# Performance work log

Measured on AMD Instinct MI355X. Metric: run time of the kernel, lower is better.

Reference implementation:

```python
import jax, jax.numpy as jnp
import numpy as np

B, T_Q, T_C = 4, 2048, 2048
Q_DIM = C_DIM = H_DIM = OUT_DIM = 1024
N_HEADS = 16
D = H_DIM // N_HEADS


def setup_inputs() -> dict:
    key = jax.random.key(0)
    ks = jax.random.split(key, 10)
    s_q = 1.0 / np.sqrt(Q_DIM)
    s_c = 1.0 / np.sqrt(C_DIM)
    s_h = 1.0 / np.sqrt(H_DIM)
    return {
        "query": jax.random.normal(ks[0], (B, T_Q, Q_DIM), jnp.float32),
        "context": jax.random.normal(ks[1], (B, T_C, C_DIM), jnp.float32),
        "Wq": jax.random.uniform(ks[2], (Q_DIM, H_DIM), jnp.float32, -s_q, s_q),
        "bq": jax.random.uniform(ks[3], (H_DIM,), jnp.float32, -s_q, s_q),
        "Wk": jax.random.uniform(ks[4], (C_DIM, H_DIM), jnp.float32, -s_c, s_c),
        "bk": jax.random.uniform(ks[5], (H_DIM,), jnp.float32, -s_c, s_c),
        "Wv": jax.random.uniform(ks[6], (C_DIM, H_DIM), jnp.float32, -s_c, s_c),
        "bv": jax.random.uniform(ks[7], (H_DIM,), jnp.float32, -s_c, s_c),
        "Wo": jax.random.uniform(ks[8], (H_DIM, OUT_DIM), jnp.float32, -s_h, s_h),
        "bo": jax.random.uniform(ks[9], (OUT_DIM,), jnp.float32, -s_h, s_h),
    }


def reference(query, context, Wq, bq, Wk, bk, Wv, bv, Wo, bo):
    Bq, Tq, _ = query.shape
    _, Tc, _ = context.shape
    # project and split heads: [B, H, T, D]
    q = (query @ Wq + bq).reshape(Bq, Tq, N_HEADS, D).transpose(0, 2, 1, 3)
    k = (context @ Wk + bk).reshape(Bq, Tc, N_HEADS, D).transpose(0, 2, 1, 3)
    v = (context @ Wv + bv).reshape(Bq, Tc, N_HEADS, D).transpose(0, 2, 1, 3)
    scores = jnp.einsum("bhqd,bhkd->bhqk", q, k) / jnp.sqrt(jnp.float32(D))
    probs = jax.nn.softmax(scores, axis=-1)
    attn = jnp.einsum("bhqk,bhkd->bhqd", probs, v)  # dropout p=0 -> identity
    attn = attn.transpose(0, 2, 1, 3).reshape(Bq, Tq, N_HEADS * D)
    return attn @ Wo + bo
```

## Files before the change

kernel.cpp:

```cpp
#include <hip/hip_runtime.h>
#include <hip/hip_bf16.h>
#include <cstdint>

typedef __attribute__((ext_vector_type(8))) short short8;
typedef __attribute__((ext_vector_type(4))) short short4_t;
typedef __attribute__((ext_vector_type(4))) float f32x4;

#define MFMA16(a, b, c) __builtin_amdgcn_mfma_f32_16x16x32_bf16(a, b, c, 0, 0, 0)

__device__ __forceinline__ short f2b(float f) {
    union { float fp; unsigned u; } un; un.fp = f;
    unsigned r = un.u + 0x7fffu + ((un.u >> 16) & 1u);
    return (short)(r >> 16);
}

#if __has_builtin(__builtin_amdgcn_cvt_pk_bf16_f32)
__device__ __forceinline__ unsigned pk_bf16(float a, float b) {
    auto r = __builtin_amdgcn_cvt_pk_bf16_f32(a, b);
    unsigned u; __builtin_memcpy(&u, &r, 4); return u;
}
#else
__device__ __forceinline__ unsigned pk_bf16(float a, float b) {
    return (unsigned)(unsigned short)f2b(a) | ((unsigned)(unsigned short)f2b(b) << 16);
}
#endif

typedef const __attribute__((address_space(1))) unsigned g_as1;
typedef __attribute__((address_space(3))) unsigned l_as3;
__device__ __forceinline__ void gll16(const ushort* g, ushort* l) {
    __builtin_amdgcn_global_load_lds((g_as1*)g, (l_as3*)l, 16, 0, 0);
}

__global__ __launch_bounds__(256) void in_cvt_kernel(
    const float* __restrict__ q, const float* __restrict__ c,
    ushort* __restrict__ qb, ushort* __restrict__ cb)
{
    const float* src = blockIdx.y ? c : q;
    ushort* dst = blockIdx.y ? cb : qb;
    size_t i = ((size_t)blockIdx.x * 256 + threadIdx.x) * 8;
    float4 v0 = *(const float4*)&src[i];
    float4 v1 = *(const float4*)&src[i + 4];
    uint4 o;
    o.x = pk_bf16(v0.x, v0.y); o.y = pk_bf16(v0.z, v0.w);
    o.z = pk_bf16(v1.x, v1.y); o.w = pk_bf16(v1.z, v1.w);
    *(uint4*)&dst[i] = o;
}

__global__ __launch_bounds__(256) void wt_cvt_kernel(
    const float* __restrict__ Wq, const float* __restrict__ Wk,
    const float* __restrict__ Wv, const float* __restrict__ Wo,
    ushort* __restrict__ wt)
{
    __shared__ float Ts[64 * 65];
    const int z = blockIdx.z;
    const float* W = (z == 0) ? Wq : (z == 1) ? Wk : (z == 2) ? Wv : Wo;
    ushort* WT = wt + (size_t)z * (1024 * 1024);
    const int n0 = blockIdx.x * 64, k0 = blockIdx.y * 64;
    const int tid = threadIdx.x;

#pragma unroll
    for (int rr = 0; rr < 4; ++rr) {
        int u = tid + rr * 256;
        int r = u >> 4, c = (u & 15) * 4;
        float4 v = *(const float4*)&W[(size_t)(k0 + r) * 1024 + n0 + c];
        Ts[r * 65 + c + 0] = v.x; Ts[r * 65 + c + 1] = v.y;
        Ts[r * 65 + c + 2] = v.z; Ts[r * 65 + c + 3] = v.w;
    }
    __syncthreads();
#pragma unroll
    for (int rr = 0; rr < 4; ++rr) {
        int u = tid + rr * 256;
        int rn = u >> 4, ck = (u & 15) * 4;
        short4_t o;
        o[0] = f2b(Ts[(ck + 0) * 65 + rn]);
        o[1] = f2b(Ts[(ck + 1) * 65 + rn]);
        o[2] = f2b(Ts[(ck + 2) * 65 + rn]);
        o[3] = f2b(Ts[(ck + 3) * 65 + rn]);
        *(short4_t*)&WT[(size_t)(n0 + rn) * 1024 + k0 + ck] = o;
    }
}

template <int MODE>
__global__ __launch_bounds__(256) void gemm_kernel(
    const ushort* __restrict__ Ag, const ushort* __restrict__ BT,
    const float* __restrict__ bias, void* __restrict__ Outp, float scale)
{
    __shared__ ushort As[128 * 64];
    __shared__ ushort Bs[128 * 64];
    const int tid = threadIdx.x;
    const int w = tid >> 6, lane = tid & 63;
    const int ln = tid & 15, quad = (tid >> 4) & 3;
    const int wm = w >> 1, wn = w & 1;
    const int m0 = blockIdx.y * 128, n0 = blockIdx.x * 128;

    int offA[4], offB[4], lseg[4];
#pragma unroll
    for (int rr = 0; rr < 4; ++rr) {
        int idx = (rr * 4 + w) * 64 + lane;
        int r = idx >> 3, cst = idx & 7, csrc = cst ^ (r & 7);
        offA[rr] = (m0 + r) * 1024 + csrc * 8;
        offB[rr] = (n0 + r) * 1024 + csrc * 8;
        lseg[rr] = (rr * 4 + w) * 512;
    }

    f32x4 acc[4][4] = {};

    for (int kk = 0; kk < 1024; kk += 64) {
        __syncthreads();
#pragma unroll
        for (int rr = 0; rr < 4; ++rr)
            gll16(&Ag[(size_t)(offA[rr] + kk)], &As[lseg[rr]]);
#pragma unroll
        for (int rr = 0; rr < 4; ++rr)
            gll16(&BT[(size_t)(offB[rr] + kk)], &Bs[lseg[rr]]);
        __syncthreads();

#pragma unroll
        for (int ks = 0; ks < 2; ++ks) {
            short8 af[4], bfr[4];
#pragma unroll
            for (int i = 0; i < 4; ++i)
                af[i] = *(const short8*)&As[(wm * 64 + i * 16 + ln) * 64 +
                                            ((ks * 4 + quad) ^ (ln & 7)) * 8];
#pragma unroll
            for (int j = 0; j < 4; ++j)
                bfr[j] = *(const short8*)&Bs[(wn * 64 + j * 16 + ln) * 64 +
                                             ((ks * 4 + quad) ^ (ln & 7)) * 8];
#pragma unroll
            for (int i = 0; i < 4; ++i)
#pragma unroll
                for (int j = 0; j < 4; ++j)
                    acc[i][j] = MFMA16(af[i], bfr[j], acc[i][j]);
        }
    }

#pragma unroll
    for (int j = 0; j < 4; ++j) {
        int n = n0 + wn * 64 + j * 16 + ln;
        float bv = bias[n];
#pragma unroll
        for (int i = 0; i < 4; ++i) {
            int mb = m0 + wm * 64 + i * 16 + quad * 4;
            if (MODE == 3) {
                float* Out = (float*)Outp;
#pragma unroll
                for (int r = 0; r < 4; ++r)
                    Out[(size_t)(mb + r) * 1024 + n] = acc[i][j][r] + bv;
            } else if (MODE == 0) {
                ushort* Out = (ushort*)Outp;
                int h = n >> 6, d = n & 63;
#pragma unroll
                for (int r = 0; r < 4; ++r) {
                    int m = mb + r, b = m >> 11, t = m & 2047;
                    Out[(((size_t)(b * 16 + h) * 2048 + t) << 6) + d] =
                        (ushort)f2b((acc[i][j][r] + bv) * scale);
                }
            } else {
                ushort* Out = (ushort*)Outp;
                int h = n >> 6, d = n & 63;
                int b = mb >> 11, t = mb & 2047;
                short4_t o;
                o[0] = f2b(acc[i][j][0] + bv); o[1] = f2b(acc[i][j][1] + bv);
                o[2] = f2b(acc[i][j][2] + bv); o[3] = f2b(acc[i][j][3] + bv);
                *(short4_t*)&Out[((size_t)((b * 16 + h) * 64 + d) << 11) + t] = o;
            }
        }
    }
}

__global__ __launch_bounds__(256, 4) void attn_kernel(
    const ushort* __restrict__ Qw, const ushort* __restrict__ Kw,
    const ushort* __restrict__ Vtw, ushort* __restrict__ attn)
{
    __shared__ ushort Ks[64 * 64];
    __shared__ ushort Vts[64 * 64];
    __shared__ ushort Ps[128 * 64];
    __shared__ float red[128];

    const int tid = threadIdx.x;
    const int w = tid >> 6, lane = tid & 63;
    const int ln = tid & 15, quad = (tid >> 4) & 3;
    const int bh = blockIdx.y, b = bh >> 4, h = bh & 15;
    const int qt = blockIdx.x;

    const ushort* Qg = Qw + (size_t)bh * 131072 + (size_t)qt * 8192;
    const ushort* Kg = Kw + (size_t)bh * 131072;
    const ushort* Vg = Vtw + (size_t)bh * 131072;

    short8 bq[2][2];
#pragma unroll
    for (int qs = 0; qs < 2; ++qs)
#pragma unroll
        for (int ks = 0; ks < 2; ++ks)
            bq[qs][ks] = *(const short8*)&Qg[(w * 32 + qs * 16 + ln) * 64 + ks * 32 + quad * 8];

    int offK[2], offV[2], lseg[2];
#pragma unroll
    for (int rr = 0; rr < 2; ++rr) {
        int idx = (rr * 4 + w) * 64 + lane;
        int r = idx >> 3, cst = idx & 7, csrc = cst ^ (r & 7);
        offK[rr] = r * 64 + csrc * 8;
        offV[rr] = r * 2048 + csrc * 8;
        lseg[rr] = (rr * 4 + w) * 512;
    }

    f32x4 Of[2][4] = {};
    float psum[2] = {0.f, 0.f};

    for (int kt = 0; kt < 32; ++kt) {
        __syncthreads();
#pragma unroll
        for (int rr = 0; rr < 2; ++rr)
            gll16(&Kg[kt * 4096 + offK[rr]], &Ks[lseg[rr]]);
#pragma unroll
        for (int rr = 0; rr < 2; ++rr)
            gll16(&Vg[kt * 64 + offV[rr]], &Vts[lseg[rr]]);
        __syncthreads();

        f32x4 sa[4][2];
#pragma unroll
        for (int kv = 0; kv < 4; ++kv) {
            short8 a0 = *(const short8*)&Ks[(kv * 16 + ln) * 64 + (quad ^ (ln & 7)) * 8];
            short8 a1 = *(const short8*)&Ks[(kv * 16 + ln) * 64 + ((4 + quad) ^ (ln & 7)) * 8];
#pragma unroll
            for (int qs = 0; qs < 2; ++qs) {
                f32x4 s = {};
                s = MFMA16(a0, bq[qs][0], s);
                s = MFMA16(a1, bq[qs][1], s);
                sa[kv][qs] = s;
            }
        }

#pragma unroll
        for (int qs = 0; qs < 2; ++qs) {
            int qrow = w * 32 + qs * 16 + ln;
#pragma unroll
            for (int kv = 0; kv < 4; ++kv) {
                float p0 = __builtin_amdgcn_exp2f(sa[kv][qs][0]);
                float p1 = __builtin_amdgcn_exp2f(sa[kv][qs][1]);
                float p2 = __builtin_amdgcn_exp2f(sa[kv][qs][2]);
                float p3 = __builtin_amdgcn_exp2f(sa[kv][qs][3]);
                psum[qs] += (p0 + p1) + (p2 + p3);
                uint2 pk2;
                pk2.x = pk_bf16(p0, p1);
                pk2.y = pk_bf16(p2, p3);
                int c = 2 * kv + (quad >> 1);
                *(uint2*)&Ps[qrow * 64 + ((c ^ (ln & 7)) * 8) + (quad & 1) * 4] = pk2;
            }
        }

#pragma unroll
        for (int ks = 0; ks < 2; ++ks) {
            short8 vb[4];
#pragma unroll
            for (int ds = 0; ds < 4; ++ds)
                vb[ds] = *(const short8*)&Vts[(ds * 16 + ln) * 64 +
                                              ((ks * 4 + quad) ^ (ln & 7)) * 8];
#pragma unroll
            for (int qs = 0; qs < 2; ++qs) {
                short8 pa = *(const short8*)&Ps[(w * 32 + qs * 16 + ln) * 64 +
                                                ((ks * 4 + quad) ^ (ln & 7)) * 8];
#pragma unroll
                for (int ds = 0; ds < 4; ++ds)
                    Of[qs][ds] = MFMA16(pa, vb[ds], Of[qs][ds]);
            }
        }
    }

#pragma unroll
    for (int qs = 0; qs < 2; ++qs) {
        float l = psum[qs];
        l += __shfl_xor(l, 16);
        l += __shfl_xor(l, 32);
        if (quad == 0) red[w * 32 + qs * 16 + ln] = __builtin_amdgcn_rcpf(l);
    }

#pragma unroll
    for (int qs = 0; qs < 2; ++qs) {
        f32x4 inv = *(const f32x4*)&red[w * 32 + qs * 16 + quad * 4];
#pragma unroll
        for (int ds = 0; ds < 4; ++ds) {
#pragma unroll
            for (int r = 0; r < 4; ++r) {
                int t = qt * 128 + w * 32 + qs * 16 + quad * 4 + r;
                int col = h * 64 + ds * 16 + ln;
                attn[((size_t)(b * 2048 + t) << 10) + col] =
                    (ushort)f2b(Of[qs][ds][r] * inv[r]);
            }
        }
    }
}

extern "C" void kernel_launch(void* const* d_in, const int* in_sizes, int n_in,
                              void* d_out, int out_size, void* d_ws, size_t ws_size,
                              hipStream_t stream)
{
    const float* query   = (const float*)d_in[0];
    const float* context = (const float*)d_in[1];
    const float* Wq = (const float*)d_in[2];
    const float* bq = (const float*)d_in[3];
    const float* Wk = (const float*)d_in[4];
    const float* bk = (const float*)d_in[5];
    const float* Wv = (const float*)d_in[6];
    const float* bv = (const float*)d_in[7];
    const float* Wo = (const float*)d_in[8];
    const float* bo = (const float*)d_in[9];

    char* ws = (char*)d_ws;
    ushort* WT  = (ushort*)ws;
    ushort* Qb  = (ushort*)(ws + 8388608);
    ushort* Qw  = (ushort*)(ws + 25165824);
    ushort* Kw  = (ushort*)(ws + 41943040);
    ushort* Vtw = (ushort*)(ws + 58720256);
    ushort* Aw  = Qb;
    ushort* Cb  = (ushort*)d_out;

    const float SCALE = 0.18033688011112042f;

    in_cvt_kernel<<<dim3(4096, 2), 256, 0, stream>>>(query, context, Qb, Cb);
    wt_cvt_kernel<<<dim3(16, 16, 4), 256, 0, stream>>>(Wq, Wk, Wv, Wo, WT);
    gemm_kernel<0><<<dim3(8, 64), 256, 0, stream>>>(Qb, WT + 0 * 1048576, bq, Qw, SCALE);
    gemm_kernel<0><<<dim3(8, 64), 256, 0, stream>>>(Cb, WT + 1 * 1048576, bk, Kw, 1.0f);
    gemm_kernel<2><<<dim3(8, 64), 256, 0, stream>>>(Cb, WT + 2 * 1048576, bv, Vtw, 1.0f);
    attn_kernel<<<dim3(16, 64), 256, 0, stream>>>(Qw, Kw, Vtw, Aw);
    gemm_kernel<3><<<dim3(8, 64), 256, 0, stream>>>(Aw, WT + 3 * 1048576, bo, d_out, 1.0f);
}
```

Before: 332.2 us.

## Double-buffer K/V tiles in attention and fuse K/V projection launches

The attention kernel now double-buffers its K and V^T shared-memory tiles. It prefetches the next tile with async global-to-LDS loads while computing on the current one, which leaves a single barrier per iteration and hides load latency. The K and V projections are merged into one kv_kernel launch that selects weights and output layout by block index, saving a launch and sharing the context input. The larger shared-memory footprint lowers the attention occupancy hint from 4 to 3 blocks, and an explicit barrier is added before reading the reduction buffer.

```diff
diff --git a/kernel.cpp b/kernel.cpp
--- a/kernel.cpp
+++ b/kernel.cpp
@@ -146,7 +146,7 @@
 #pragma unroll
                 for (int r = 0; r < 4; ++r)
                     Out[(size_t)(mb + r) * 1024 + n] = acc[i][j][r] + bv;
-            } else if (MODE == 0) {
+            } else {
                 ushort* Out = (ushort*)Outp;
                 int h = n >> 6, d = n & 63;
 #pragma unroll
@@ -155,25 +155,106 @@
                     Out[(((size_t)(b * 16 + h) * 2048 + t) << 6) + d] =
                         (ushort)f2b((acc[i][j][r] + bv) * scale);
                 }
-            } else {
-                ushort* Out = (ushort*)Outp;
-                int h = n >> 6, d = n & 63;
+            }
+        }
+    }
+}
+
+__global__ __launch_bounds__(256) void kv_kernel(
+    const ushort* __restrict__ Cb, const ushort* __restrict__ WTk,
+    const ushort* __restrict__ WTv,
+    const float* __restrict__ bk, const float* __restrict__ bv,
+    ushort* __restrict__ Kw, ushort* __restrict__ Vtw)
+{
+    __shared__ ushort As[128 * 64];
+    __shared__ ushort Bs[128 * 64];
+    const int tid = threadIdx.x;
+    const int w = tid >> 6, lane = tid & 63;
+    const int ln = tid & 15, quad = (tid >> 4) & 3;
+    const int wm = w >> 1, wn = w & 1;
+    const int z = blockIdx.x >> 3;
+    const int n0 = (blockIdx.x & 7) * 128;
+    const int m0 = blockIdx.y * 128;
+    const ushort* BT = z ? WTv : WTk;
+
+    int offA[4], offB[4], lseg[4];
+#pragma unroll
+    for (int rr = 0; rr < 4; ++rr) {
+        int idx = (rr * 4 + w) * 64 + lane;
+        int r = idx >> 3, cst = idx & 7, csrc = cst ^ (r & 7);
+        offA[rr] = (m0 + r) * 1024 + csrc * 8;
+        offB[rr] = (n0 + r) * 1024 + csrc * 8;
+        lseg[rr] = (rr * 4 + w) * 512;
+    }
+
+    f32x4 acc[4][4] = {};
+
+    for (int kk = 0; kk < 1024; kk += 64) {
+        __syncthreads();
+#pragma unroll
+        for (int rr = 0; rr < 4; ++rr)
+            gll16(&Cb[(size_t)(offA[rr] + kk)], &As[lseg[rr]]);
+#pragma unroll
+        for (int rr = 0; rr < 4; ++rr)
+            gll16(&BT[(size_t)(offB[rr] + kk)], &Bs[lseg[rr]]);
+        __syncthreads();
+
+#pragma unroll
+        for (int ks = 0; ks < 2; ++ks) {
+            short8 af[4], bfr[4];
+#pragma unroll
+            for (int i = 0; i < 4; ++i)
+                af[i] = *(const short8*)&As[(wm * 64 + i * 16 + ln) * 64 +
+                                            ((ks * 4 + quad) ^ (ln & 7)) * 8];
+#pragma unroll
+            for (int j = 0; j < 4; ++j)
+                bfr[j] = *(const short8*)&Bs[(wn * 64 + j * 16 + ln) * 64 +
+                                             ((ks * 4 + quad) ^ (ln & 7)) * 8];
+#pragma unroll
+            for (int i = 0; i < 4; ++i)
+#pragma unroll
+                for (int j = 0; j < 4; ++j)
+                    acc[i][j] = MFMA16(af[i], bfr[j], acc[i][j]);
+        }
+    }
+
+#pragma unroll
+    for (int j = 0; j < 4; ++j) {
+        int n = n0 + wn * 64 + j * 16 + ln;
+        int h = n >> 6, d = n & 63;
+        if (z == 0) {
+            float bvv = bk[n];
+#pragma unroll
+            for (int i = 0; i < 4; ++i) {
+                int mb = m0 + wm * 64 + i * 16 + quad * 4;
+#pragma unroll
+                for (int r = 0; r < 4; ++r) {
+                    int m = mb + r, b = m >> 11, t = m & 2047;
+                    Kw[(((size_t)(b * 16 + h) * 2048 + t) << 6) + d] =
+                        (ushort)f2b(acc[i][j][r] + bvv);
+                }
+            }
+        } else {
+            float bvv = bv[n];
+#pragma unroll
+            for (int i = 0; i < 4; ++i) {
+                int mb = m0 + wm * 64 + i * 16 + quad * 4;
                 int b = mb >> 11, t = mb & 2047;
                 short4_t o;
-                o[0] = f2b(acc[i][j][0] + bv); o[1] = f2b(acc[i][j][1] + bv);
-                o[2] = f2b(acc[i][j][2] + bv); o[3] = f2b(acc[i][j][3] + bv);
-                *(short4_t*)&Out[((size_t)((b * 16 + h) * 64 + d) << 11) + t] = o;
-            }
-        }
-    }
-}
-
-__global__ __launch_bounds__(256, 4) void attn_kernel(
+                o[0] = f2b(acc[i][j][0] + bvv); o[1] = f2b(acc[i][j][1] + bvv);
+                o[2] = f2b(acc[i][j][2] + bvv); o[3] = f2b(acc[i][j][3] + bvv);
+                *(short4_t*)&Vtw[(((size_t)((b * 16 + h) * 64 + d)) << 11) + t] = o;
+            }
+        }
+    }
+}
+
+__global__ __launch_bounds__(256, 3) void attn_kernel(
     const ushort* __restrict__ Qw, const ushort* __restrict__ Kw,
     const ushort* __restrict__ Vtw, ushort* __restrict__ attn)
 {
-    __shared__ ushort Ks[64 * 64];
-    __shared__ ushort Vts[64 * 64];
+    __shared__ ushort Ks[2 * 4096];
+    __shared__ ushort Vts[2 * 4096];
     __shared__ ushort Ps[128 * 64];
     __shared__ float red[128];
 
@@ -204,24 +285,34 @@
         lseg[rr] = (rr * 4 + w) * 512;
     }
 
+#pragma unroll
+    for (int rr = 0; rr < 2; ++rr) gll16(&Kg[offK[rr]], &Ks[lseg[rr]]);
+#pragma unroll
+    for (int rr = 0; rr < 2; ++rr) gll16(&Vg[offV[rr]], &Vts[lseg[rr]]);
+
     f32x4 Of[2][4] = {};
     float psum[2] = {0.f, 0.f};
 
     for (int kt = 0; kt < 32; ++kt) {
         __syncthreads();
-#pragma unroll
-        for (int rr = 0; rr < 2; ++rr)
-            gll16(&Kg[kt * 4096 + offK[rr]], &Ks[lseg[rr]]);
-#pragma unroll
-        for (int rr = 0; rr < 2; ++rr)
-            gll16(&Vg[kt * 64 + offV[rr]], &Vts[lseg[rr]]);
-        __syncthreads();
+        const int cur = (kt & 1) * 4096;
+        if (kt < 31) {
+            const int nx = 4096 - cur;
+#pragma unroll
+            for (int rr = 0; rr < 2; ++rr)
+                gll16(&Kg[(kt + 1) * 4096 + offK[rr]], &Ks[nx + lseg[rr]]);
+#pragma unroll
+            for (int rr = 0; rr < 2; ++rr)
+                gll16(&Vg[(kt + 1) * 64 + offV[rr]], &Vts[nx + lseg[rr]]);
+        }
+        const ushort* ksm = &Ks[cur];
+        const ushort* vsm = &Vts[cur];
 
         f32x4 sa[4][2];
 #pragma unroll
         for (int kv = 0; kv < 4; ++kv) {
-            short8 a0 = *(const short8*)&Ks[(kv * 16 + ln) * 64 + (quad ^ (ln & 7)) * 8];
-            short8 a1 = *(const short8*)&Ks[(kv * 16 + ln) * 64 + ((4 + quad) ^ (ln & 7)) * 8];
+            short8 a0 = *(const short8*)&ksm[(kv * 16 + ln) * 64 + (quad ^ (ln & 7)) * 8];
+            short8 a1 = *(const short8*)&ksm[(kv * 16 + ln) * 64 + ((4 + quad) ^ (ln & 7)) * 8];
 #pragma unroll
             for (int qs = 0; qs < 2; ++qs) {
                 f32x4 s = {};
@@ -251,19 +342,20 @@
 
 #pragma unroll
         for (int ks = 0; ks < 2; ++ks) {
-            short8 vb[4];
+            short8 vb[4], pa[2];
 #pragma unroll
             for (int ds = 0; ds < 4; ++ds)
-                vb[ds] = *(const short8*)&Vts[(ds * 16 + ln) * 64 +
+                vb[ds] = *(const short8*)&vsm[(ds * 16 + ln) * 64 +
                                               ((ks * 4 + quad) ^ (ln & 7)) * 8];
 #pragma unroll
-            for (int qs = 0; qs < 2; ++qs) {
-                short8 pa = *(const short8*)&Ps[(w * 32 + qs * 16 + ln) * 64 +
-                                                ((ks * 4 + quad) ^ (ln & 7)) * 8];
+            for (int qs = 0; qs < 2; ++qs)
+                pa[qs] = *(const short8*)&Ps[(w * 32 + qs * 16 + ln) * 64 +
+                                             ((ks * 4 + quad) ^ (ln & 7)) * 8];
+#pragma unroll
+            for (int qs = 0; qs < 2; ++qs)
 #pragma unroll
                 for (int ds = 0; ds < 4; ++ds)
-                    Of[qs][ds] = MFMA16(pa, vb[ds], Of[qs][ds]);
-            }
+                    Of[qs][ds] = MFMA16(pa[qs], vb[ds], Of[qs][ds]);
         }
     }
 
@@ -274,6 +366,7 @@
         l += __shfl_xor(l, 32);
         if (quad == 0) red[w * 32 + qs * 16 + ln] = __builtin_amdgcn_rcpf(l);
     }
+    __syncthreads();
 
 #pragma unroll
     for (int qs = 0; qs < 2; ++qs) {
@@ -320,8 +413,9 @@
     in_cvt_kernel<<<dim3(4096, 2), 256, 0, stream>>>(query, context, Qb, Cb);
     wt_cvt_kernel<<<dim3(16, 16, 4), 256, 0, stream>>>(Wq, Wk, Wv, Wo, WT);
     gemm_kernel<0><<<dim3(8, 64), 256, 0, stream>>>(Qb, WT + 0 * 1048576, bq, Qw, SCALE);
-    gemm_kernel<0><<<dim3(8, 64), 256, 0, stream>>>(Cb, WT + 1 * 1048576, bk, Kw, 1.0f);
-    gemm_kernel<2><<<dim3(8, 64), 256, 0, stream>>>(Cb, WT + 2 * 1048576, bv, Vtw, 1.0f);
+    kv_kernel<<<dim3(16, 64), 256, 0, stream>>>(Cb, WT + 1 * 1048576,
+                                                WT + 2 * 1048576, bk, bv, Kw, Vtw);
     attn_kernel<<<dim3(16, 64), 256, 0, stream>>>(Qw, Kw, Vtw, Aw);
-    gemm_kernel<3><<<dim3(8, 64), 256, 0, stream>>>(Aw, WT + 3 * 1048576, bo, d_out, 1.0f);
-}
+    gemm_kernel<3><<<dim3(8, 64), 256, 0, stream>>>(Aw, WT + 3 * 1048576, bo,
+                                                    (float*)d_out, 1.0f);
+}
```

Result: no change. 329.3 us (-0.9%).
